# Optimization experiments

Measured on AMD Instinct MI355X. Metric: run time of the kernel, lower is better.

Reference implementation:

```python
import jax, jax.numpy as jnp
import numpy as np

N_INT4, N_INT8, K, GROUP = 6144, 2048, 8192, 128
N_TOTAL = N_INT4 + N_INT8
M = 16


def setup_inputs() -> dict:
    key = jax.random.key(0)
    ks = jax.random.split(key, 8)
    x = jax.random.normal(ks[0], (M, K), jnp.float32)
    # uint4 weights: values 0..15 (stored int32)
    w_int4 = jax.random.randint(ks[1], (N_INT4, K), 0, 16, jnp.int32)
    # group-wise scales [N_int4, K//group_size]
    s_int4 = jax.random.uniform(ks[2], (N_INT4, K // GROUP), jnp.float32, minval=0.005, maxval=0.02)
    # int8 weights stored in offset-128 form (w_int8 + 128 -> 0..255), as pack_for_marlin builds
    w_uint8 = jax.random.randint(ks[3], (N_INT8, K), 0, 256, jnp.int32)
    # per-channel int8 scales
    s_int8 = jax.random.uniform(ks[4], (N_INT8,), jnp.float32, minval=0.005, maxval=0.02)
    awq_scales = jax.random.uniform(ks[5], (K,), jnp.float32, minval=0.5, maxval=2.0)
    bias = jax.random.normal(ks[6], (N_TOTAL,), jnp.float32) * 0.01
    inv_perm = jax.random.permutation(ks[7], N_TOTAL).astype(jnp.int32)
    return dict(x=x, w_int4=w_int4, s_int4=s_int4, w_uint8=w_uint8, s_int8=s_int8,
                awq_scales=awq_scales, bias=bias, inv_perm=inv_perm, group_size=GROUP)


def reference(x, w_int4, s_int4, w_uint8, s_int8, awq_scales, bias, inv_perm, group_size):
    dt = x.dtype
    k = x.shape[-1]
    # AWQ input scaling (unfused path: x / awq_scales)
    x2 = x.reshape(-1, k) / awq_scales[None, :]
    sum_x = jnp.sum(x2, axis=1, keepdims=True)  # [M, 1]

    # Marlin uint4b8 dequant: (q - 8) * scale, group-wise scales for int4 rows
    s4_k = jnp.repeat(s_int4, group_size, axis=1)            # [N4, K]
    W4 = (w_int4.astype(dt) - 8.0) * s4_k                    # [N4, K]

    # int8 rows split into high/low nibbles with scales 16*s and s
    high = (w_uint8 >> 4) & 15
    low = w_uint8 & 15
    Wh = (high.astype(dt) - 8.0) * (16.0 * s_int8)[:, None]  # [N8, K]
    Wl = (low.astype(dt) - 8.0) * s_int8[:, None]            # [N8, K]

    Wc = jnp.concatenate([W4, Wh, Wl], axis=0)               # [N4+2*N8, K]
    y = x2 @ Wc.T                                            # marlin_gemm equivalent

    n4 = W4.shape[0]
    n8 = s_int8.shape[0]
    y4 = y[:, :n4]
    # int8 reconstruction: y_high + y_low + 8*s_int8*sum_x  == s_int8 * (x @ w_int8^T)
    y8 = y[:, n4:n4 + n8] + y[:, n4 + n8:] + (8.0 * s_int8)[None, :] * sum_x
    y_out = jnp.concatenate([y4, y8], axis=-1)[:, inv_perm] + bias[None, :]
    return y_out.reshape(*x.shape[:-1], n4 + n8)
```

## Files before the change

kernel.cpp:

```cpp
#include <hip/hip_runtime.h>
#include <hip/hip_bf16.h>

constexpr int K    = 8192;
constexpr int N4   = 6144;
constexpr int N8   = 2048;
constexpr int NT   = N4 + N8;
constexpr int NG   = K / 128;
constexpr int KS   = 4096;

typedef short  short8  __attribute__((ext_vector_type(8)));
typedef float  floatx4 __attribute__((ext_vector_type(4)));

__device__ inline short f2bf(float f) {
    __hip_bfloat16 h = __float2bfloat16(f);
    return __builtin_bit_cast(short, h);
}

__global__ void prep_kernel(const float* __restrict__ x,
                            const float* __restrict__ awq,
                            const int*   __restrict__ inv_perm,
                            const float* __restrict__ bias,
                            short* __restrict__ x2bf,
                            int*   __restrict__ fwd,
                            float* __restrict__ out) {
    const int tid  = blockIdx.x * blockDim.x + threadIdx.x;
    const int c    = tid >> 9;
    const int rem  = tid & 511;
    const int lane = rem >> 3;
    const int j    = rem & 7;
    const int m    = lane & 15;
    const int k    = c * 32 + (lane >> 4) * 8 + j;
    x2bf[tid] = f2bf(x[m * K + k] / awq[k]);
    if (tid < NT) fwd[inv_perm[tid]] = tid;
    out[tid] = bias[tid & (NT - 1)];
}

__global__ __launch_bounds__(256, 4)
void qgemv_kernel(const short* __restrict__ xf,
                  const int*   __restrict__ w4,
                  const float* __restrict__ s4,
                  const int*   __restrict__ w8,
                  const float* __restrict__ s8,
                  const int*   __restrict__ fwd,
                  float* __restrict__ out) {
    __shared__ float lds[4 * 256];

    const int t     = threadIdx.x;
    const int lane  = t & 63;
    const int w     = t >> 6;
    const int tile  = blockIdx.x >> 1;
    const int split = blockIdx.x & 1;
    const int nb    = tile * 16;
    const int i     = lane & 15;
    const int q     = lane >> 4;
    const int row   = nb + i;

    const bool is4  = (nb < N4);
    const int kbase = split * KS + w * 1024;
    const int*   wp = (is4 ? (w4 + (size_t)row * K)
                           : (w8 + (size_t)(row - N4) * K))
                      + kbase + q * 8;
    const short* xw = xf + (size_t)(kbase >> 5) * 512 + lane * 8;
    const float* sp = is4 ? (s4 + (size_t)row * NG + (kbase >> 7)) : nullptr;

    floatx4 acc = {0.f, 0.f, 0.f, 0.f};

    int4   wbA[8], wbB[8];
    short8 abA[4], abB[4];
    float  sA = 0.f, sB = 0.f;

    auto loadg = [&](int g, int4* wb, short8* ab, float& s) {
        #pragma unroll
        for (int c = 0; c < 4; ++c) {
            const size_t co = (size_t)(g * 4 + c);
            wb[2 * c]     = *(const int4*)(wp + co * 32);
            wb[2 * c + 1] = *(const int4*)(wp + co * 32 + 4);
            ab[c]         = *(const short8*)(xw + co * 512);
        }
        if (is4) s = sp[g];
    };

    auto compg = [&](const int4* wb, const short8* ab, float s) {
        const float sc = is4 ? s : 1.f;
        const float sb = is4 ? -8.f * s : -128.f;
        #pragma unroll
        for (int c = 0; c < 4; ++c) {
            const int4 wa = wb[2 * c];
            const int4 wz = wb[2 * c + 1];
            short8 bf;
            bf[0] = f2bf((float)wa.x * sc + sb);
            bf[1] = f2bf((float)wa.y * sc + sb);
            bf[2] = f2bf((float)wa.z * sc + sb);
            bf[3] = f2bf((float)wa.w * sc + sb);
            bf[4] = f2bf((float)wz.x * sc + sb);
            bf[5] = f2bf((float)wz.y * sc + sb);
            bf[6] = f2bf((float)wz.z * sc + sb);
            bf[7] = f2bf((float)wz.w * sc + sb);
            acc = __builtin_amdgcn_mfma_f32_16x16x32_bf16(ab[c], bf, acc, 0, 0, 0);
        }
    };

    loadg(0, wbA, abA, sA);
    __builtin_amdgcn_sched_barrier(0);
    #pragma unroll 1
    for (int g = 0; g < 6; g += 2) {
        loadg(g + 1, wbB, abB, sB);
        __builtin_amdgcn_sched_barrier(0);
        compg(wbA, abA, sA);
        loadg(g + 2, wbA, abA, sA);
        __builtin_amdgcn_sched_barrier(0);
        compg(wbB, abB, sB);
    }
    loadg(7, wbB, abB, sB);
    __builtin_amdgcn_sched_barrier(0);
    compg(wbA, abA, sA);
    compg(wbB, abB, sB);

    #pragma unroll
    for (int r = 0; r < 4; ++r)
        lds[w * 256 + (q * 4 + r) * 16 + i] = acc[r];
    __syncthreads();

    {
        const int m  = t >> 4;
        const int i2 = t & 15;
        const float v = lds[0 * 256 + t] + lds[1 * 256 + t]
                      + lds[2 * 256 + t] + lds[3 * 256 + t];
        const int n  = nb + i2;
        const float sc = is4 ? 1.f : s8[n - N4];
        const int d  = fwd[n];
        atomicAdd(&out[(size_t)m * NT + d], v * sc);
    }
}

extern "C" void kernel_launch(void* const* d_in, const int* in_sizes, int n_in,
                              void* d_out, int out_size, void* d_ws, size_t ws_size,
                              hipStream_t stream) {
    const float* x        = (const float*)d_in[0];
    const int*   w_int4   = (const int*)  d_in[1];
    const float* s_int4   = (const float*)d_in[2];
    const int*   w_uint8  = (const int*)  d_in[3];
    const float* s_int8   = (const float*)d_in[4];
    const float* awq      = (const float*)d_in[5];
    const float* bias     = (const float*)d_in[6];
    const int*   inv_perm = (const int*)  d_in[7];

    short* x2bf = (short*)d_ws;
    int*   fwd  = (int*)((char*)d_ws + (size_t)16 * K * sizeof(short));

    prep_kernel<<<(16 * K) / 256, 256, 0, stream>>>(x, awq, inv_perm, bias,
                                                    x2bf, fwd, (float*)d_out);
    qgemv_kernel<<<(NT / 16) * 2, 256, 0, stream>>>(x2bf, w_int4, s_int4,
                                                    w_uint8, s_int8, fwd,
                                                    (float*)d_out);
}
```

Before: 336.7 us.

## Stage weight tiles into LDS via direct global-to-LDS loads with double buffering

Replaces per-thread register-prefetched weight loads with a cooperative scheme. Each wave issues global_load_lds for four full rows of a 256-wide K tile into a double-buffered LDS area, then all waves read the weights they need from LDS for the MFMA dequant path. The aim is fully coalesced row-contiguous global reads and lower register pressure, so the kernel can hide latency with buffered staging. In exchange it adds two block-level barriers per K step and LDS traffic, and it drops the occupancy hint from launch bounds.

```diff
diff --git a/kernel.cpp b/kernel.cpp
--- a/kernel.cpp
+++ b/kernel.cpp
@@ -1,12 +1,15 @@
 #include <hip/hip_runtime.h>
 #include <hip/hip_bf16.h>
 
-constexpr int K    = 8192;
-constexpr int N4   = 6144;
-constexpr int N8   = 2048;
-constexpr int NT   = N4 + N8;
-constexpr int NG   = K / 128;
-constexpr int KS   = 4096;
+constexpr int K     = 8192;
+constexpr int N4    = 6144;
+constexpr int N8    = 2048;
+constexpr int NT    = N4 + N8;
+constexpr int NG    = K / 128;
+constexpr int KS    = 4096;
+constexpr int KT    = 256;
+constexpr int NSTEP = KS / KT;
+constexpr int ROWB  = KT * 4 + 16;
 
 typedef short  short8  __attribute__((ext_vector_type(8)));
 typedef float  floatx4 __attribute__((ext_vector_type(4)));
@@ -14,6 +17,12 @@
 __device__ inline short f2bf(float f) {
     __hip_bfloat16 h = __float2bfloat16(f);
     return __builtin_bit_cast(short, h);
+}
+
+__device__ inline void gload_lds16(const void* g, void* l) {
+    __builtin_amdgcn_global_load_lds(
+        (const __attribute__((address_space(1))) void*)g,
+        (__attribute__((address_space(3))) void*)l, 16, 0, 0);
 }
 
 __global__ void prep_kernel(const float* __restrict__ x,
@@ -35,7 +44,7 @@
     out[tid] = bias[tid & (NT - 1)];
 }
 
-__global__ __launch_bounds__(256, 4)
+__global__ __launch_bounds__(256)
 void qgemv_kernel(const short* __restrict__ xf,
                   const int*   __restrict__ w4,
                   const float* __restrict__ s4,
@@ -43,7 +52,7 @@
                   const float* __restrict__ s8,
                   const int*   __restrict__ fwd,
                   float* __restrict__ out) {
-    __shared__ float lds[4 * 256];
+    __shared__ __align__(16) char ldsbuf[2 * 16 * ROWB];
 
     const int t     = threadIdx.x;
     const int lane  = t & 63;
@@ -53,40 +62,63 @@
     const int nb    = tile * 16;
     const int i     = lane & 15;
     const int q     = lane >> 4;
-    const int row   = nb + i;
+    const bool is4  = (nb < N4);
 
-    const bool is4  = (nb < N4);
-    const int kbase = split * KS + w * 1024;
-    const int*   wp = (is4 ? (w4 + (size_t)row * K)
-                           : (w8 + (size_t)(row - N4) * K))
-                      + kbase + q * 8;
-    const short* xw = xf + (size_t)(kbase >> 5) * 512 + lane * 8;
-    const float* sp = is4 ? (s4 + (size_t)row * NG + (kbase >> 7)) : nullptr;
+    const int kbase = split * KS;
 
+    const int r0 = w * 4;
+    const int* rowp0; const int* rowp1; const int* rowp2; const int* rowp3;
+    {
+        const int rg = nb + r0;
+        const int* b0 = is4 ? (w4 + (size_t)rg * K)
+                            : (w8 + (size_t)(rg - N4) * K);
+        rowp0 = b0 + kbase;
+        rowp1 = b0 + (size_t)K + kbase;
+        rowp2 = b0 + (size_t)2 * K + kbase;
+        rowp3 = b0 + (size_t)3 * K + kbase;
+    }
+
+    const short* xbase = xf + (size_t)(split * 128) * 512 + lane * 8;
+    const float* sp = is4 ? (s4 + (size_t)(nb + i) * NG + split * 32 + (w >> 1))
+                          : nullptr;
+
+    const int c0 = w * 2;
     floatx4 acc = {0.f, 0.f, 0.f, 0.f};
 
-    int4   wbA[8], wbB[8];
-    short8 abA[4], abB[4];
-    float  sA = 0.f, sB = 0.f;
-
-    auto loadg = [&](int g, int4* wb, short8* ab, float& s) {
-        #pragma unroll
-        for (int c = 0; c < 4; ++c) {
-            const size_t co = (size_t)(g * 4 + c);
-            wb[2 * c]     = *(const int4*)(wp + co * 32);
-            wb[2 * c + 1] = *(const int4*)(wp + co * 32 + 4);
-            ab[c]         = *(const short8*)(xw + co * 512);
-        }
-        if (is4) s = sp[g];
+    auto STAGE = [&](int tt, int b) {
+        char* lb = ldsbuf + b * (16 * ROWB) + r0 * ROWB;
+        const int ko = tt * KT + lane * 4;
+        gload_lds16(rowp0 + ko, lb);
+        gload_lds16(rowp1 + ko, lb + ROWB);
+        gload_lds16(rowp2 + ko, lb + 2 * ROWB);
+        gload_lds16(rowp3 + ko, lb + 3 * ROWB);
     };
 
-    auto compg = [&](const int4* wb, const short8* ab, float s) {
-        const float sc = is4 ? s : 1.f;
-        const float sb = is4 ? -8.f * s : -128.f;
+    STAGE(0, 0);
+
+    #pragma unroll 1
+    for (int tt = 0; tt < NSTEP; ++tt) {
+        const int b = tt & 1;
+        const short8 xa = *(const short8*)(xbase + (size_t)(tt * 8 + c0) * 512);
+        const short8 xb = *(const short8*)(xbase + (size_t)(tt * 8 + c0 + 1) * 512);
+        float sv = 0.f;
+        if (is4) sv = sp[tt * 2];
+        __builtin_amdgcn_sched_barrier(0);
+        if (tt + 1 < NSTEP) STAGE(tt + 1, b ^ 1);
+        __builtin_amdgcn_sched_barrier(0);
+        if (tt + 1 < NSTEP) asm volatile("s_waitcnt vmcnt(4)" ::: "memory");
+        else                asm volatile("s_waitcnt vmcnt(0)" ::: "memory");
+        __builtin_amdgcn_sched_barrier(0);
+        __builtin_amdgcn_s_barrier();
+
+        const float sc = is4 ? sv : 1.f;
+        const float sb = is4 ? -8.f * sv : -128.f;
+        const char* lrow = ldsbuf + b * (16 * ROWB) + i * ROWB + q * 32;
         #pragma unroll
-        for (int c = 0; c < 4; ++c) {
-            const int4 wa = wb[2 * c];
-            const int4 wz = wb[2 * c + 1];
+        for (int c2 = 0; c2 < 2; ++c2) {
+            const char* lb2 = lrow + (c0 + c2) * 128;
+            const int4 wa = *(const int4*)lb2;
+            const int4 wz = *(const int4*)(lb2 + 16);
             short8 bf;
             bf[0] = f2bf((float)wa.x * sc + sb);
             bf[1] = f2bf((float)wa.y * sc + sb);
@@ -96,40 +128,28 @@
             bf[5] = f2bf((float)wz.y * sc + sb);
             bf[6] = f2bf((float)wz.z * sc + sb);
             bf[7] = f2bf((float)wz.w * sc + sb);
-            acc = __builtin_amdgcn_mfma_f32_16x16x32_bf16(ab[c], bf, acc, 0, 0, 0);
+            acc = __builtin_amdgcn_mfma_f32_16x16x32_bf16(c2 ? xb : xa, bf, acc,
+                                                          0, 0, 0);
         }
-    };
+        __builtin_amdgcn_sched_barrier(0);
+        __builtin_amdgcn_s_barrier();
+    }
 
-    loadg(0, wbA, abA, sA);
-    __builtin_amdgcn_sched_barrier(0);
-    #pragma unroll 1
-    for (int g = 0; g < 6; g += 2) {
-        loadg(g + 1, wbB, abB, sB);
-        __builtin_amdgcn_sched_barrier(0);
-        compg(wbA, abA, sA);
-        loadg(g + 2, wbA, abA, sA);
-        __builtin_amdgcn_sched_barrier(0);
-        compg(wbB, abB, sB);
-    }
-    loadg(7, wbB, abB, sB);
-    __builtin_amdgcn_sched_barrier(0);
-    compg(wbA, abA, sA);
-    compg(wbB, abB, sB);
-
+    float* red = (float*)ldsbuf;
     #pragma unroll
     for (int r = 0; r < 4; ++r)
-        lds[w * 256 + (q * 4 + r) * 16 + i] = acc[r];
+        red[w * 256 + (q * 4 + r) * 16 + i] = acc[r];
     __syncthreads();
 
     {
         const int m  = t >> 4;
         const int i2 = t & 15;
-        const float v = lds[0 * 256 + t] + lds[1 * 256 + t]
-                      + lds[2 * 256 + t] + lds[3 * 256 + t];
+        const float v = red[0 * 256 + t] + red[1 * 256 + t]
+                      + red[2 * 256 + t] + red[3 * 256 + t];
         const int n  = nb + i2;
-        const float sc = is4 ? 1.f : s8[n - N4];
+        const float scd = is4 ? 1.f : s8[n - N4];
         const int d  = fwd[n];
-        atomicAdd(&out[(size_t)m * NT + d], v * sc);
+        atomicAdd(&out[(size_t)m * NT + d], v * scd);
     }
 }
 
```

Result: no change. 339.3 us (+0.8%).

## Repack int32 weights into nibble/byte-packed layout before the quantized GEMV

Applied to the files above, without the earlier changes.

Adds a repack kernel that compresses the int32-stored uint4 and uint8 weights into packed 32-bit words, ordered to match the MFMA fragment layout. The GEMV then loads one or two uint4 vectors per group instead of eight int4 vectors, and unpacks with shifts and masks. This cuts the memory traffic and load instructions inside the GEMV, but the full int32 weights are still read once per call by the repack pass, plus an extra write and re-read of the packed data. The occupancy hint on the GEMV launch bounds is also dropped.

```diff
diff --git a/kernel.cpp b/kernel.cpp
--- a/kernel.cpp
+++ b/kernel.cpp
@@ -7,6 +7,11 @@
 constexpr int NT   = N4 + N8;
 constexpr int NG   = K / 128;
 constexpr int KS   = 4096;
+
+constexpr int P4_ROWD = K / 8;
+constexpr int P8_ROWD = K / 4;
+constexpr int P4_DWORDS = N4 * P4_ROWD;
+constexpr int P8_DWORDS = N8 * P8_ROWD;
 
 typedef short  short8  __attribute__((ext_vector_type(8)));
 typedef float  floatx4 __attribute__((ext_vector_type(4)));
@@ -35,11 +40,50 @@
     out[tid] = bias[tid & (NT - 1)];
 }
 
-__global__ __launch_bounds__(256, 4)
+__global__ __launch_bounds__(256)
+void repack_kernel(const int* __restrict__ w4, const int* __restrict__ w8,
+                   unsigned int* __restrict__ p4, unsigned int* __restrict__ p8) {
+    const int t = blockIdx.x * 256 + threadIdx.x;
+    if (t < P4_DWORDS) {
+        const int r   = t >> 10;
+        const int d   = t & 1023;
+        const int G   = d >> 4;
+        const int rem = d & 15;
+        const int q   = rem >> 2;
+        const int c   = rem & 3;
+        const int kk  = G * 128 + c * 32 + q * 8;
+        const int* src = w4 + (size_t)r * K + kk;
+        const int4 a = *(const int4*)src;
+        const int4 b = *(const int4*)(src + 4);
+        unsigned int v = (unsigned int)a.x        | ((unsigned int)a.y << 4)
+                       | ((unsigned int)a.z << 8) | ((unsigned int)a.w << 12)
+                       | ((unsigned int)b.x << 16)| ((unsigned int)b.y << 20)
+                       | ((unsigned int)b.z << 24)| ((unsigned int)b.w << 28);
+        p4[t] = v;
+    } else {
+        const int t8  = t - P4_DWORDS;
+        const int r   = t8 >> 11;
+        const int d   = t8 & 2047;
+        const int G   = d >> 5;
+        const int rem = d & 31;
+        const int q   = rem >> 3;
+        const int c   = (rem >> 1) & 3;
+        const int h   = rem & 1;
+        const int kk  = G * 128 + c * 32 + q * 8 + h * 4;
+        const int4 a = *(const int4*)(w8 + (size_t)r * K + kk);
+        unsigned int v = (unsigned int)(a.x & 255)
+                       | ((unsigned int)(a.y & 255) << 8)
+                       | ((unsigned int)(a.z & 255) << 16)
+                       | ((unsigned int)(a.w & 255) << 24);
+        p8[t8] = v;
+    }
+}
+
+__global__ __launch_bounds__(256)
 void qgemv_kernel(const short* __restrict__ xf,
-                  const int*   __restrict__ w4,
+                  const unsigned int* __restrict__ p4,
                   const float* __restrict__ s4,
-                  const int*   __restrict__ w8,
+                  const unsigned int* __restrict__ p8,
                   const float* __restrict__ s8,
                   const int*   __restrict__ fwd,
                   float* __restrict__ out) {
@@ -54,67 +98,81 @@
     const int i     = lane & 15;
     const int q     = lane >> 4;
     const int row   = nb + i;
-
     const bool is4  = (nb < N4);
-    const int kbase = split * KS + w * 1024;
-    const int*   wp = (is4 ? (w4 + (size_t)row * K)
-                           : (w8 + (size_t)(row - N4) * K))
-                      + kbase + q * 8;
-    const short* xw = xf + (size_t)(kbase >> 5) * 512 + lane * 8;
-    const float* sp = is4 ? (s4 + (size_t)row * NG + (kbase >> 7)) : nullptr;
+    const int row8  = is4 ? 0 : (row - N4);
+    const int G0    = split * 32 + w * 8;
+
+    const unsigned int* wp4 = p4 + (size_t)row  * P4_ROWD + G0 * 16 + q * 4;
+    const unsigned int* wp8 = p8 + (size_t)row8 * P8_ROWD + G0 * 32 + q * 8;
+    const short* xw = xf + (size_t)G0 * 4 * 512 + lane * 8;
+    const float* sp = is4 ? (s4 + (size_t)row * NG + G0) : nullptr;
 
     floatx4 acc = {0.f, 0.f, 0.f, 0.f};
 
-    int4   wbA[8], wbB[8];
-    short8 abA[4], abB[4];
+    uint4  w4A, w4B;
+    uint4  w8A[2], w8B[2];
+    short8 xA[4], xB[4];
     float  sA = 0.f, sB = 0.f;
 
-    auto loadg = [&](int g, int4* wb, short8* ab, float& s) {
+    auto loadg = [&](int g, uint4& wv4, uint4* wv8, short8* xv, float& s) {
+        if (is4) {
+            wv4 = *(const uint4*)(wp4 + (size_t)g * 16);
+            s   = sp[g];
+        } else {
+            wv8[0] = *(const uint4*)(wp8 + (size_t)g * 32);
+            wv8[1] = *(const uint4*)(wp8 + (size_t)g * 32 + 4);
+        }
         #pragma unroll
-        for (int c = 0; c < 4; ++c) {
-            const size_t co = (size_t)(g * 4 + c);
-            wb[2 * c]     = *(const int4*)(wp + co * 32);
-            wb[2 * c + 1] = *(const int4*)(wp + co * 32 + 4);
-            ab[c]         = *(const short8*)(xw + co * 512);
-        }
-        if (is4) s = sp[g];
+        for (int c = 0; c < 4; ++c)
+            xv[c] = *(const short8*)(xw + (size_t)(g * 4 + c) * 512);
     };
 
-    auto compg = [&](const int4* wb, const short8* ab, float s) {
-        const float sc = is4 ? s : 1.f;
-        const float sb = is4 ? -8.f * s : -128.f;
-        #pragma unroll
-        for (int c = 0; c < 4; ++c) {
-            const int4 wa = wb[2 * c];
-            const int4 wz = wb[2 * c + 1];
-            short8 bf;
-            bf[0] = f2bf((float)wa.x * sc + sb);
-            bf[1] = f2bf((float)wa.y * sc + sb);
-            bf[2] = f2bf((float)wa.z * sc + sb);
-            bf[3] = f2bf((float)wa.w * sc + sb);
-            bf[4] = f2bf((float)wz.x * sc + sb);
-            bf[5] = f2bf((float)wz.y * sc + sb);
-            bf[6] = f2bf((float)wz.z * sc + sb);
-            bf[7] = f2bf((float)wz.w * sc + sb);
-            acc = __builtin_amdgcn_mfma_f32_16x16x32_bf16(ab[c], bf, acc, 0, 0, 0);
+    auto compg = [&](const uint4& wv4, const uint4* wv8, const short8* xv,
+                     float s) {
+        if (is4) {
+            const float sc = s, sb = -8.f * s;
+            #pragma unroll
+            for (int c = 0; c < 4; ++c) {
+                const unsigned int v = wv4[c];
+                short8 bf;
+                #pragma unroll
+                for (int j = 0; j < 8; ++j)
+                    bf[j] = f2bf((float)((v >> (4 * j)) & 15u) * sc + sb);
+                acc = __builtin_amdgcn_mfma_f32_16x16x32_bf16(xv[c], bf, acc,
+                                                              0, 0, 0);
+            }
+        } else {
+            #pragma unroll
+            for (int c = 0; c < 4; ++c) {
+                const unsigned int lo = (c < 2 ? wv8[0] : wv8[1])[(c & 1) * 2];
+                const unsigned int hi = (c < 2 ? wv8[0] : wv8[1])[(c & 1) * 2 + 1];
+                short8 bf;
+                #pragma unroll
+                for (int j = 0; j < 4; ++j) {
+                    bf[j]     = f2bf((float)((lo >> (8 * j)) & 255u) - 128.f);
+                    bf[4 + j] = f2bf((float)((hi >> (8 * j)) & 255u) - 128.f);
+                }
+                acc = __builtin_amdgcn_mfma_f32_16x16x32_bf16(xv[c], bf, acc,
+                                                              0, 0, 0);
+            }
         }
     };
 
-    loadg(0, wbA, abA, sA);
+    loadg(0, w4A, w8A, xA, sA);
     __builtin_amdgcn_sched_barrier(0);
     #pragma unroll 1
     for (int g = 0; g < 6; g += 2) {
-        loadg(g + 1, wbB, abB, sB);
+        loadg(g + 1, w4B, w8B, xB, sB);
         __builtin_amdgcn_sched_barrier(0);
-        compg(wbA, abA, sA);
-        loadg(g + 2, wbA, abA, sA);
+        compg(w4A, w8A, xA, sA);
+        loadg(g + 2, w4A, w8A, xA, sA);
         __builtin_amdgcn_sched_barrier(0);
-        compg(wbB, abB, sB);
+        compg(w4B, w8B, xB, sB);
     }
-    loadg(7, wbB, abB, sB);
+    loadg(7, w4B, w8B, xB, sB);
     __builtin_amdgcn_sched_barrier(0);
-    compg(wbA, abA, sA);
-    compg(wbB, abB, sB);
+    compg(w4A, w8A, xA, sA);
+    compg(w4B, w8B, xB, sB);
 
     #pragma unroll
     for (int r = 0; r < 4; ++r)
@@ -145,12 +203,18 @@
     const float* bias     = (const float*)d_in[6];
     const int*   inv_perm = (const int*)  d_in[7];
 
-    short* x2bf = (short*)d_ws;
-    int*   fwd  = (int*)((char*)d_ws + (size_t)16 * K * sizeof(short));
+    char* ws = (char*)d_ws;
+    short* x2bf       = (short*)ws;
+    int*   fwd        = (int*)(ws + 256 * 1024);
+    unsigned int* p4  = (unsigned int*)(ws + 512 * 1024);
+    unsigned int* p8  = (unsigned int*)(ws + 512 * 1024
+                                        + (size_t)P4_DWORDS * 4);
 
     prep_kernel<<<(16 * K) / 256, 256, 0, stream>>>(x, awq, inv_perm, bias,
                                                     x2bf, fwd, (float*)d_out);
-    qgemv_kernel<<<(NT / 16) * 2, 256, 0, stream>>>(x2bf, w_int4, s_int4,
-                                                    w_uint8, s_int8, fwd,
+    repack_kernel<<<(P4_DWORDS + P8_DWORDS) / 256, 256, 0, stream>>>(
+        w_int4, w_uint8, p4, p8);
+    qgemv_kernel<<<(NT / 16) * 2, 256, 0, stream>>>(x2bf, p4, s_int4,
+                                                    p8, s_int8, fwd,
                                                     (float*)d_out);
 }
```

After: 354.9 us. 1.05x slower.
